# Performance work log

Measured on AMD Instinct MI355X. Metric: run time of the kernel, lower is better.

Reference implementation:

```python
import jax, jax.numpy as jnp
import numpy as np

B, IN, OUT = 64, 1024, 1024

def setup_inputs() -> dict:
    key = jax.random.key(0)
    ks = jax.random.split(key, 7)
    return {
        "x": jax.random.normal(ks[0], (B, IN), dtype=jnp.float32),
        "mu": jax.random.normal(ks[1], (IN, OUT), dtype=jnp.float32),
        "ro": jax.random.normal(ks[2], (IN, OUT), dtype=jnp.float32),
        "mu_bias": jax.random.normal(ks[3], (1, OUT), dtype=jnp.float32),
        "ro_bias": jax.random.normal(ks[4], (1, OUT), dtype=jnp.float32),
        "eps": jax.random.normal(ks[5], (B, IN, OUT), dtype=jnp.float32),
        "eps_bias": jax.random.normal(ks[6], (B, OUT), dtype=jnp.float32),
    }

def reference(x, mu, ro, mu_bias, ro_bias, eps, eps_bias):
    # sigma = log(1 + exp(ro))  (softplus), same for bias
    sigma = jax.nn.softplus(ro)            # [IN, OUT]
    sigma_bias = jax.nn.softplus(ro_bias)  # [1, OUT]
    weights = eps * sigma + mu             # [B, IN, OUT] per-sample weights
    bias = eps_bias * sigma_bias + mu_bias # [B, OUT]
    # batched matvec: x[b,i] @ weights[b,i,o] -> [B, OUT]
    out = jnp.einsum("bi,bio->bo", x, weights) + bias
    return out
```

## Files before the change

### kernel.cpp

```cpp
#include <hip/hip_runtime.h>


#define BB   64
#define INN  1024
#define OUTT 1024
#define B_T  4
#define ICH  32
#define I_C  (INN / ICH)

typedef float f4 __attribute__((ext_vector_type(4)));

__device__ __forceinline__ float softplus_f(float v) {
    return fmaxf(v, 0.0f) + log1pf(__expf(-fabsf(v)));
}

__global__ __launch_bounds__(256) void bayes_sig(
    const float* __restrict__ ro, float* __restrict__ sig)
{
    const int g = blockIdx.x * 256 + threadIdx.x;
    const f4 r = *(const f4*)(ro + (size_t)g * 4);
    f4 s;
    s.x = softplus_f(r.x); s.y = softplus_f(r.y);
    s.z = softplus_f(r.z); s.w = softplus_f(r.w);
    *(f4*)(sig + (size_t)g * 4) = s;
}

__global__ __launch_bounds__(256) void bayes_main(
    const float* __restrict__ x,
    const float* __restrict__ mu,
    const float* __restrict__ sig,
    const float* __restrict__ eps,
    float* __restrict__ part)
{
    __shared__ float xs[B_T][I_C];

    const int t  = threadIdx.x;
    const int o  = t << 2;
    const int c  = blockIdx.x;
    const int b0 = blockIdx.y * B_T;
    const int i0 = c * I_C;

    if (t < B_T * I_C) {
        const int b  = t / I_C;
        const int il = t % I_C;
        xs[b][il] = x[(b0 + b) * INN + i0 + il];
    }
    __syncthreads();

    f4 acc[B_T];
#pragma unroll
    for (int b = 0; b < B_T; ++b) acc[b] = (f4)0.0f;

#pragma unroll 4
    for (int il = 0; il < I_C; ++il) {
        const int i = i0 + il;
        const f4 sg4 = *(const f4*)(sig + (size_t)i * OUTT + o);
        const f4 mu4 = *(const f4*)(mu  + (size_t)i * OUTT + o);
#pragma unroll
        for (int b = 0; b < B_T; ++b) {
            const float xb = xs[b][il];
            const f4 e = __builtin_nontemporal_load(
                (const f4*)(eps + ((size_t)(b0 + b) * INN + i) * OUTT + o));
            acc[b].x = fmaf(xb, fmaf(e.x, sg4.x, mu4.x), acc[b].x);
            acc[b].y = fmaf(xb, fmaf(e.y, sg4.y, mu4.y), acc[b].y);
            acc[b].z = fmaf(xb, fmaf(e.z, sg4.z, mu4.z), acc[b].z);
            acc[b].w = fmaf(xb, fmaf(e.w, sg4.w, mu4.w), acc[b].w);
        }
    }

#pragma unroll
    for (int b = 0; b < B_T; ++b) {
        *(f4*)(part + ((size_t)(b0 + b) * ICH + c) * OUTT + o) = acc[b];
    }
}

__global__ __launch_bounds__(256) void bayes_reduce(
    const float* __restrict__ part,
    const float* __restrict__ mu_bias,
    const float* __restrict__ ro_bias,
    const float* __restrict__ eps_bias,
    float* __restrict__ out)
{
    const int g  = blockIdx.x * 256 + threadIdx.x;
    const int b  = g >> 8;
    const int o  = (g & 255) << 2;

    f4 s = (f4)0.0f;
#pragma unroll
    for (int c = 0; c < ICH; ++c) {
        const f4 p = *(const f4*)(part + ((size_t)b * ICH + c) * OUTT + o);
        s.x += p.x; s.y += p.y; s.z += p.z; s.w += p.w;
    }

    const f4 rb = *(const f4*)(ro_bias + o);
    const f4 mb = *(const f4*)(mu_bias + o);
    const f4 eb = *(const f4*)(eps_bias + (size_t)b * OUTT + o);
    s.x += fmaf(eb.x, softplus_f(rb.x), mb.x);
    s.y += fmaf(eb.y, softplus_f(rb.y), mb.y);
    s.z += fmaf(eb.z, softplus_f(rb.z), mb.z);
    s.w += fmaf(eb.w, softplus_f(rb.w), mb.w);

    *(f4*)(out + (size_t)g * 4) = s;
}

__global__ __launch_bounds__(256) void bayes_mono(
    const float* __restrict__ x, const float* __restrict__ mu,
    const float* __restrict__ ro, const float* __restrict__ mu_bias,
    const float* __restrict__ ro_bias, const float* __restrict__ eps,
    const float* __restrict__ eps_bias, float* __restrict__ out)
{
    const int t = threadIdx.x;
    const int o = t << 2;
    const int b = blockIdx.x;

    f4 acc = (f4)0.0f;
    for (int i = 0; i < INN; ++i) {
        const float xb = x[b * INN + i];
        const f4 r4 = *(const f4*)(ro + (size_t)i * OUTT + o);
        const f4 m4 = *(const f4*)(mu + (size_t)i * OUTT + o);
        const f4 e  = *(const f4*)(eps + ((size_t)b * INN + i) * OUTT + o);
        acc.x = fmaf(xb, fmaf(e.x, softplus_f(r4.x), m4.x), acc.x);
        acc.y = fmaf(xb, fmaf(e.y, softplus_f(r4.y), m4.y), acc.y);
        acc.z = fmaf(xb, fmaf(e.z, softplus_f(r4.z), m4.z), acc.z);
        acc.w = fmaf(xb, fmaf(e.w, softplus_f(r4.w), m4.w), acc.w);
    }
    const f4 rb = *(const f4*)(ro_bias + o);
    const f4 mb = *(const f4*)(mu_bias + o);
    const f4 eb = *(const f4*)(eps_bias + (size_t)b * OUTT + o);
    acc.x += fmaf(eb.x, softplus_f(rb.x), mb.x);
    acc.y += fmaf(eb.y, softplus_f(rb.y), mb.y);
    acc.z += fmaf(eb.z, softplus_f(rb.z), mb.z);
    acc.w += fmaf(eb.w, softplus_f(rb.w), mb.w);
    *(f4*)(out + (size_t)b * OUTT + o) = acc;
}

extern "C" void kernel_launch(void* const* d_in, const int* in_sizes, int n_in,
                              void* d_out, int out_size, void* d_ws, size_t ws_size,
                              hipStream_t stream) {
    const float* x        = (const float*)d_in[0];
    const float* mu       = (const float*)d_in[1];
    const float* ro       = (const float*)d_in[2];
    const float* mu_bias  = (const float*)d_in[3];
    const float* ro_bias  = (const float*)d_in[4];
    const float* eps      = (const float*)d_in[5];
    const float* eps_bias = (const float*)d_in[6];
    float* out = (float*)d_out;

    const size_t sig_elems  = (size_t)INN * OUTT;
    const size_t part_elems = (size_t)BB * ICH * OUTT;
    const size_t need = (sig_elems + part_elems) * sizeof(float);

    if (ws_size >= need) {
        float* sig  = (float*)d_ws;
        float* part = sig + sig_elems;

        bayes_sig<<<sig_elems / 1024, 256, 0, stream>>>(ro, sig);
        dim3 grid(ICH, BB / B_T);
        bayes_main<<<grid, 256, 0, stream>>>(x, mu, sig, eps, part);
        bayes_reduce<<<(BB * OUTT / 4) / 256, 256, 0, stream>>>(
            part, mu_bias, ro_bias, eps_bias, out);
    } else {
        bayes_mono<<<BB, 256, 0, stream>>>(x, mu, ro, mu_bias, ro_bias,
                                           eps, eps_bias, out);
    }
}
```

Baseline: 369.4 us.

## Fuse softplus into main kernel and double input-dimension split

Removes the separate sigma precompute kernel and computes softplus of ro inline in the main matvec loop, which drops one launch and the write and reread of a sigma buffer. It also doubles the number of input chunks to launch more blocks, and switches eps loads from nontemporal to normal loads. The cost is redundant softplus work across batch tiles and a larger partial-sum buffer for the reduce kernel to read.

```diff
diff --git a/kernel.cpp b/kernel.cpp
--- a/kernel.cpp
+++ b/kernel.cpp
@@ -5,7 +5,7 @@
 #define INN  1024
 #define OUTT 1024
 #define B_T  4
-#define ICH  32
+#define ICH  64
 #define I_C  (INN / ICH)
 
 typedef float f4 __attribute__((ext_vector_type(4)));
@@ -14,21 +14,10 @@
     return fmaxf(v, 0.0f) + log1pf(__expf(-fabsf(v)));
 }
 
-__global__ __launch_bounds__(256) void bayes_sig(
-    const float* __restrict__ ro, float* __restrict__ sig)
-{
-    const int g = blockIdx.x * 256 + threadIdx.x;
-    const f4 r = *(const f4*)(ro + (size_t)g * 4);
-    f4 s;
-    s.x = softplus_f(r.x); s.y = softplus_f(r.y);
-    s.z = softplus_f(r.z); s.w = softplus_f(r.w);
-    *(f4*)(sig + (size_t)g * 4) = s;
-}
-
 __global__ __launch_bounds__(256) void bayes_main(
     const float* __restrict__ x,
     const float* __restrict__ mu,
-    const float* __restrict__ sig,
+    const float* __restrict__ ro,
     const float* __restrict__ eps,
     float* __restrict__ part)
 {
@@ -54,13 +43,17 @@
 #pragma unroll 4
     for (int il = 0; il < I_C; ++il) {
         const int i = i0 + il;
-        const f4 sg4 = *(const f4*)(sig + (size_t)i * OUTT + o);
-        const f4 mu4 = *(const f4*)(mu  + (size_t)i * OUTT + o);
+        const f4 ro4 = *(const f4*)(ro + (size_t)i * OUTT + o);
+        const f4 mu4 = *(const f4*)(mu + (size_t)i * OUTT + o);
+        f4 sg4;
+        sg4.x = softplus_f(ro4.x);
+        sg4.y = softplus_f(ro4.y);
+        sg4.z = softplus_f(ro4.z);
+        sg4.w = softplus_f(ro4.w);
 #pragma unroll
         for (int b = 0; b < B_T; ++b) {
             const float xb = xs[b][il];
-            const f4 e = __builtin_nontemporal_load(
-                (const f4*)(eps + ((size_t)(b0 + b) * INN + i) * OUTT + o));
+            const f4 e = *(const f4*)(eps + ((size_t)(b0 + b) * INN + i) * OUTT + o);
             acc[b].x = fmaf(xb, fmaf(e.x, sg4.x, mu4.x), acc[b].x);
             acc[b].y = fmaf(xb, fmaf(e.y, sg4.y, mu4.y), acc[b].y);
             acc[b].z = fmaf(xb, fmaf(e.z, sg4.z, mu4.z), acc[b].z);
@@ -86,7 +79,7 @@
     const int o  = (g & 255) << 2;
 
     f4 s = (f4)0.0f;
-#pragma unroll
+#pragma unroll 8
     for (int c = 0; c < ICH; ++c) {
         const f4 p = *(const f4*)(part + ((size_t)b * ICH + c) * OUTT + o);
         s.x += p.x; s.y += p.y; s.z += p.z; s.w += p.w;
@@ -146,17 +139,14 @@
     const float* eps_bias = (const float*)d_in[6];
     float* out = (float*)d_out;
 
-    const size_t sig_elems  = (size_t)INN * OUTT;
     const size_t part_elems = (size_t)BB * ICH * OUTT;
-    const size_t need = (sig_elems + part_elems) * sizeof(float);
+    const size_t need = part_elems * sizeof(float);
 
     if (ws_size >= need) {
-        float* sig  = (float*)d_ws;
-        float* part = sig + sig_elems;
+        float* part = (float*)d_ws;
 
-        bayes_sig<<<sig_elems / 1024, 256, 0, stream>>>(ro, sig);
         dim3 grid(ICH, BB / B_T);
-        bayes_main<<<grid, 256, 0, stream>>>(x, mu, sig, eps, part);
+        bayes_main<<<grid, 256, 0, stream>>>(x, mu, ro, eps, part);
         bayes_reduce<<<(BB * OUTT / 4) / 256, 256, 0, stream>>>(
             part, mu_bias, ro_bias, eps_bias, out);
     } else {
```

Result: slower. 389.1 us (+5.3%).
